# Kernel optimization log

Measured on AMD Instinct MI355X. Metric: run time of the kernel, lower is better.

Reference implementation:

```python
import jax, jax.numpy as jnp
import numpy as np
import math

LOG2 = math.log(2.0)
N, AGENT, STATE, COMA, UNITS = 2048, 5, 128, 64, 32

def setup_inputs() -> dict:
    key = jax.random.key(0)
    k1, k2, k3, k4, k5, k6 = jax.random.split(key, 6)
    state = jax.random.normal(k1, (N, AGENT, STATE), dtype=jnp.float32)
    joint_action = jax.random.normal(k2, (N, AGENT, COMA), dtype=jnp.float32)
    # Linear params (stored [in, out]); torch default init ~ U(-1/sqrt(in), 1/sqrt(in))
    s1 = 1.0 / math.sqrt(STATE)
    s2 = 1.0 / math.sqrt(COMA)
    W1 = jax.random.uniform(k3, (STATE, UNITS), jnp.float32, -s1, s1)
    b1 = jax.random.uniform(k4, (UNITS,), jnp.float32, -s1, s1)
    W2 = jax.random.uniform(k5, (COMA, UNITS), jnp.float32, -s2, s2)
    b2 = jax.random.uniform(k6, (UNITS,), jnp.float32, -s2, s2)
    return {"state": state, "joint_action": joint_action,
            "W1": W1, "b1": b1, "W2": W2, "b2": b2}

def reference(state, joint_action, W1, b1, W2, b2):
    # dual embeddings: Linear -> leaky_relu (default negative_slope=0.01)
    em1 = jax.nn.leaky_relu(state @ W1 + b1)          # [N, A, U]
    em2 = jax.nn.leaky_relu(joint_action @ W2 + b2)   # [N, A, U]
    n, a, _ = em1.shape
    l = em1.reshape(n * a, UNITS)
    m = em2.reshape(n * a, UNITS)
    u = m @ l.T                                       # [N*A, N*A]
    # vectorized 5x5 block-mean pooling (replaces torch double loop)
    u = u.reshape(n, a, n, a).mean(axis=(1, 3))       # [N, N]
    # JSD measure
    sp = jax.nn.softplus(-u)
    E_pos = LOG2 - sp                                 # positive expectation
    E_neg = sp + u - LOG2                             # negative expectation
    mask = jnp.eye(n, dtype=u.dtype)
    E_pos_term = (E_pos * mask).sum(axis=1)           # diag of E_pos
    E_neg_term = (E_neg * (1.0 - mask)).sum(axis=1) / (n - 1)
    loss = E_neg_term - E_pos_term
    MI = E_pos_term
    return loss, MI
```

## Files before the change

### kernel.cpp

```cpp
#include <hip/hip_runtime.h>
#include <hip/hip_bf16.h>

#define NN 2048
#define AGENT 5
#define STATE 128
#define COMA 64
#define UNITS 32
#define LOG2F_C 0.6931471805599453f

typedef __attribute__((ext_vector_type(8))) _Float16 half8;
typedef __attribute__((ext_vector_type(4))) float f32x4;

__global__ __launch_bounds__(256) void embed_kernel(
    const float* __restrict__ state, const float* __restrict__ action,
    const float* __restrict__ W1, const float* __restrict__ b1,
    const float* __restrict__ W2, const float* __restrict__ b2,
    _Float16* __restrict__ Lh, _Float16* __restrict__ Mh) {
  int tid = blockIdx.x * 256 + threadIdx.x;
  int which = tid >> 16;
  int t = tid & 65535;
  int i = t >> 5;
  int k = t & 31;
  if (which == 0) {
    float acc = 0.f;
    float bb = b1[k];
    const float* s = state + i * (AGENT * STATE);
    for (int a = 0; a < AGENT; ++a, s += STATE) {
      float d = bb;
      #pragma unroll
      for (int c = 0; c < STATE; ++c) d = fmaf(s[c], W1[c * UNITS + k], d);
      acc += (d > 0.f) ? d : 0.01f * d;
    }
    Lh[i * UNITS + k] = (_Float16)(acc * 0.2f);
  } else {
    float acc = 0.f;
    float bb = b2[k];
    const float* s = action + i * (AGENT * COMA);
    for (int a = 0; a < AGENT; ++a, s += COMA) {
      float d = bb;
      #pragma unroll
      for (int c = 0; c < COMA; ++c) d = fmaf(s[c], W2[c * UNITS + k], d);
      acc += (d > 0.f) ? d : 0.01f * d;
    }
    Mh[i * UNITS + k] = (_Float16)(acc * 0.2f);
  }
}

__global__ __launch_bounds__(256) void pair_kernel(
    const _Float16* __restrict__ Lh, const _Float16* __restrict__ Mh,
    float* __restrict__ S, float* __restrict__ Ud) {
  int w = threadIdx.x >> 6;
  int l = threadIdx.x & 63;
  int ln15 = l & 15;
  int quad = l >> 4;
  int i0 = blockIdx.y * 64 + w * 16;
  int col0 = blockIdx.x * 256;

  half8 afrag = *(const half8*)(Mh + (i0 + ln15) * UNITS + quad * 8);

  f32x4 accs = {0.f, 0.f, 0.f, 0.f};

  for (int tile = 0; tile < 16; ++tile) {
    int j0 = col0 + tile * 16;
    half8 bfrag = *(const half8*)(Lh + (j0 + ln15) * UNITS + quad * 8);
    f32x4 c = {0.f, 0.f, 0.f, 0.f};
    c = __builtin_amdgcn_mfma_f32_16x16x32_f16(afrag, bfrag, c, 0, 0, 0);
    int gcol = j0 + ln15;
    #pragma unroll
    for (int r = 0; r < 4; ++r) {
      float u = c[r];
      int grow = i0 + quad * 4 + r;
      float sp0 = __logf(1.f + __expf(-fabsf(u)));
      float en = sp0 + fmaxf(u, 0.f) - LOG2F_C;
      accs[r] += en;
      if (grow == gcol) Ud[grow] = u;
    }
  }

  #pragma unroll
  for (int d = 1; d < 16; d <<= 1) {
    #pragma unroll
    for (int r = 0; r < 4; ++r) accs[r] += __shfl_xor(accs[r], d, 64);
  }
  if (ln15 == 0) {
    #pragma unroll
    for (int r = 0; r < 4; ++r) atomicAdd(&S[i0 + quad * 4 + r], accs[r]);
  }
}

__global__ __launch_bounds__(256) void final_kernel(
    const float* __restrict__ S, const float* __restrict__ Ud,
    float* __restrict__ out) {
  int i = blockIdx.x * 256 + threadIdx.x;
  if (i < NN) {
    float u = Ud[i];
    float sp0 = __logf(1.f + __expf(-fabsf(u)));
    float spu = sp0 + fmaxf(u, 0.f);
    float en_ii = spu - LOG2F_C;
    float sp_neg = spu - u;
    float mi = LOG2F_C - sp_neg;
    out[i] = (S[i] - en_ii) * (1.f / (NN - 1)) - mi;
    out[NN + i] = mi;
  }
}

extern "C" void kernel_launch(void* const* d_in, const int* in_sizes, int n_in,
                              void* d_out, int out_size, void* d_ws, size_t ws_size,
                              hipStream_t stream) {
  const float* state  = (const float*)d_in[0];
  const float* action = (const float*)d_in[1];
  const float* W1     = (const float*)d_in[2];
  const float* b1     = (const float*)d_in[3];
  const float* W2     = (const float*)d_in[4];
  const float* b2     = (const float*)d_in[5];

  char* w = (char*)d_ws;
  _Float16* Lh = (_Float16*)w;
  _Float16* Mh = (_Float16*)(w + 131072);
  float* S     = (float*)(w + 262144);
  float* Ud    = (float*)(w + 262144 + 8192);
  float* out   = (float*)d_out;

  hipMemsetAsync(S, 0, NN * sizeof(float), stream);

  embed_kernel<<<512, 256, 0, stream>>>(state, action, W1, b1, W2, b2, Lh, Mh);

  pair_kernel<<<dim3(8, 32), 256, 0, stream>>>(Lh, Mh, S, Ud);

  final_kernel<<<8, 256, 0, stream>>>(S, Ud, out);
}
```

Measured before the change: 88.61 us.

## Restructure embedding loops, fold memset into embed kernel, widen pair grid

The embedding kernel now loads state/action rows as float4 and keeps five per-agent accumulators, so each weight load is reused across all agents instead of reloaded per agent. The separate memset of S is folded into the embed kernel, which removes one launch. The pair kernel grid grows fourfold, with each block covering 64 columns instead of 256, to raise parallelism across CUs. The trade-off is four times as many atomicAdds into S.

```diff
diff --git a/kernel.cpp b/kernel.cpp
--- a/kernel.cpp
+++ b/kernel.cpp
@@ -15,34 +15,61 @@
     const float* __restrict__ state, const float* __restrict__ action,
     const float* __restrict__ W1, const float* __restrict__ b1,
     const float* __restrict__ W2, const float* __restrict__ b2,
-    _Float16* __restrict__ Lh, _Float16* __restrict__ Mh) {
+    _Float16* __restrict__ Lh, _Float16* __restrict__ Mh,
+    float* __restrict__ S) {
   int tid = blockIdx.x * 256 + threadIdx.x;
+  if (tid < NN) S[tid] = 0.f;
   int which = tid >> 16;
   int t = tid & 65535;
   int i = t >> 5;
   int k = t & 31;
   if (which == 0) {
-    float acc = 0.f;
     float bb = b1[k];
-    const float* s = state + i * (AGENT * STATE);
-    for (int a = 0; a < AGENT; ++a, s += STATE) {
-      float d = bb;
+    float acc[AGENT];
+    #pragma unroll
+    for (int a = 0; a < AGENT; ++a) acc[a] = bb;
+    const float4* sp = (const float4*)(state + i * (AGENT * STATE));
+    #pragma unroll 4
+    for (int c4 = 0; c4 < STATE / 4; ++c4) {
+      float4 sv[AGENT];
       #pragma unroll
-      for (int c = 0; c < STATE; ++c) d = fmaf(s[c], W1[c * UNITS + k], d);
-      acc += (d > 0.f) ? d : 0.01f * d;
+      for (int a = 0; a < AGENT; ++a) sv[a] = sp[a * (STATE / 4) + c4];
+      #pragma unroll
+      for (int j = 0; j < 4; ++j) {
+        float wv = W1[(c4 * 4 + j) * UNITS + k];
+        acc[0] = fmaf(sv[0].x * 0 + (&sv[0].x)[j], wv, acc[0]);
+        acc[1] = fmaf((&sv[1].x)[j], wv, acc[1]);
+        acc[2] = fmaf((&sv[2].x)[j], wv, acc[2]);
+        acc[3] = fmaf((&sv[3].x)[j], wv, acc[3]);
+        acc[4] = fmaf((&sv[4].x)[j], wv, acc[4]);
+      }
     }
-    Lh[i * UNITS + k] = (_Float16)(acc * 0.2f);
+    float r = 0.f;
+    #pragma unroll
+    for (int a = 0; a < AGENT; ++a) r += (acc[a] > 0.f) ? acc[a] : 0.01f * acc[a];
+    Lh[i * UNITS + k] = (_Float16)(r * 0.2f);
   } else {
-    float acc = 0.f;
     float bb = b2[k];
-    const float* s = action + i * (AGENT * COMA);
-    for (int a = 0; a < AGENT; ++a, s += COMA) {
-      float d = bb;
+    float acc[AGENT];
+    #pragma unroll
+    for (int a = 0; a < AGENT; ++a) acc[a] = bb;
+    const float4* sp = (const float4*)(action + i * (AGENT * COMA));
+    #pragma unroll 4
+    for (int c4 = 0; c4 < COMA / 4; ++c4) {
+      float4 sv[AGENT];
       #pragma unroll
-      for (int c = 0; c < COMA; ++c) d = fmaf(s[c], W2[c * UNITS + k], d);
-      acc += (d > 0.f) ? d : 0.01f * d;
+      for (int a = 0; a < AGENT; ++a) sv[a] = sp[a * (COMA / 4) + c4];
+      #pragma unroll
+      for (int j = 0; j < 4; ++j) {
+        float wv = W2[(c4 * 4 + j) * UNITS + k];
+        #pragma unroll
+        for (int a = 0; a < AGENT; ++a) acc[a] = fmaf((&sv[a].x)[j], wv, acc[a]);
+      }
     }
-    Mh[i * UNITS + k] = (_Float16)(acc * 0.2f);
+    float r = 0.f;
+    #pragma unroll
+    for (int a = 0; a < AGENT; ++a) r += (acc[a] > 0.f) ? acc[a] : 0.01f * acc[a];
+    Mh[i * UNITS + k] = (_Float16)(r * 0.2f);
   }
 }
 
@@ -54,13 +81,14 @@
   int ln15 = l & 15;
   int quad = l >> 4;
   int i0 = blockIdx.y * 64 + w * 16;
-  int col0 = blockIdx.x * 256;
+  int col0 = blockIdx.x * 64;
 
   half8 afrag = *(const half8*)(Mh + (i0 + ln15) * UNITS + quad * 8);
 
   f32x4 accs = {0.f, 0.f, 0.f, 0.f};
 
-  for (int tile = 0; tile < 16; ++tile) {
+  #pragma unroll
+  for (int tile = 0; tile < 4; ++tile) {
     int j0 = col0 + tile * 16;
     half8 bfrag = *(const half8*)(Lh + (j0 + ln15) * UNITS + quad * 8);
     f32x4 c = {0.f, 0.f, 0.f, 0.f};
@@ -121,11 +149,9 @@
   float* Ud    = (float*)(w + 262144 + 8192);
   float* out   = (float*)d_out;
 
-  hipMemsetAsync(S, 0, NN * sizeof(float), stream);
+  embed_kernel<<<512, 256, 0, stream>>>(state, action, W1, b1, W2, b2, Lh, Mh, S);
 
-  embed_kernel<<<512, 256, 0, stream>>>(state, action, W1, b1, W2, b2, Lh, Mh);
-
-  pair_kernel<<<dim3(8, 32), 256, 0, stream>>>(Lh, Mh, S, Ud);
+  pair_kernel<<<dim3(32, 32), 256, 0, stream>>>(Lh, Mh, S, Ud);
 
   final_kernel<<<8, 256, 0, stream>>>(S, Ud, out);
 }
```

New measurement: 83.65 us. -5.6%, faster.
